# Kernel tuning notes

Hardware: AMD Instinct MI355X
Metric: run time of the kernel (lower is better)

## Reference

```python
import jax, jax.numpy as jnp
import numpy as np

B, LTMS, TTS, C_IN, F, H = 64, 16, 256, 128, 256, 256


def setup_inputs() -> dict:
    key = jax.random.key(0)
    ks = jax.random.split(key, 6)
    s = 0.05  # small init keeps relu-GRU numerically tame
    return {
        "x": jax.random.normal(ks[0], (B, LTMS * TTS, C_IN), dtype=jnp.float32),
        "conv_w": jax.random.normal(ks[1], (1, C_IN, F), dtype=jnp.float32) * s,
        "conv_b": jnp.zeros((F,), dtype=jnp.float32),
        "attn_w": jax.random.normal(ks[2], (TTS, TTS), dtype=jnp.float32) * s,
        "attn_b": jnp.zeros((TTS,), dtype=jnp.float32),
        "gru_w": jax.random.normal(ks[3], (F, 3 * H), dtype=jnp.float32) * s,
        "gru_u": jax.random.normal(ks[4], (H, 3 * H), dtype=jnp.float32) * s,
        "gru_b": jnp.zeros((2, 3 * H), dtype=jnp.float32),
    }


def _forward(x, conv_w, conv_b, attn_w, attn_b, gru_w, gru_u, gru_b):
    b = x.shape[0]
    # [B, LTMS*TTS, C] -> [B*LTMS, TTS, C]; segments are independent, so the
    # original per-segment Python loop vectorizes into the leading batch dim.
    xs = x.reshape(b * LTMS, TTS, C_IN)
    # Conv1D kernel_size=1 == pointwise GEMM, then ReLU (dropout=0 at inference)
    conv = jax.nn.relu(jnp.einsum('ntc,cf->ntf', xs, conv_w[0]) + conv_b)  # [N,T,F]
    # Attention: softmax(Dense) over time axis per filter, multiply back
    xt = conv.transpose(0, 2, 1)                                  # [N,F,T]
    probs = jax.nn.softmax(xt @ attn_w + attn_b, axis=-1)         # [N,F,T]
    x_att = conv * probs.transpose(0, 2, 1)                       # [N,T,F]
    # GRU (keras v2, reset_after=True), activation=relu, gate order z,r,h
    bi, br = gru_b[0], gru_b[1]
    gates_x = x_att @ gru_w + bi                                  # [N,T,3H]
    def step(h, gx):
        rec = h @ gru_u + br
        xz, xr, xh = jnp.split(gx, 3, axis=-1)
        rz, rr, rh = jnp.split(rec, 3, axis=-1)
        z = jax.nn.sigmoid(xz + rz)
        r = jax.nn.sigmoid(xr + rr)
        hh = jax.nn.relu(xh + r * rh)
        h_new = z * h + (1.0 - z) * hh
        return h_new, None
    h0 = jnp.zeros((b * LTMS, H), dtype=x.dtype)
    h_final, _ = jax.lax.scan(step, h0, gates_x.transpose(1, 0, 2))
    return h_final.reshape(b, LTMS, H)


def reference(x, conv_w, conv_b, attn_w, attn_b, gru_w, gru_u, gru_b):
    return _forward(x, conv_w, conv_b, attn_w, attn_b, gru_w, gru_u, gru_b)
```

## Files before the change

kernel.cpp:

```cpp
#include <hip/hip_runtime.h>
#include <stdint.h>

typedef unsigned short u16;
typedef __attribute__((ext_vector_type(8))) __bf16 bf16x8;
typedef __attribute__((ext_vector_type(4))) float f32x4;

#define TTS 256
#define NSEG 1024
#define TC 32

__device__ __forceinline__ u16 f2bf(float f) {
  union { float f; uint32_t u; } v; v.f = f;
  uint32_t r = v.u + 0x7fffu + ((v.u >> 16) & 1u);
  return (u16)(r >> 16);
}
__device__ __forceinline__ float bf2f(u16 h) {
  union { uint32_t u; float f; } v; v.u = ((uint32_t)h) << 16;
  return v.f;
}
__device__ __forceinline__ float sigm(float x) {
  return __builtin_amdgcn_rcpf(1.0f + __expf(-x));
}
__device__ __forceinline__ void gl16(const void* g, void* l) {
  __builtin_amdgcn_global_load_lds(
      (const __attribute__((address_space(1))) unsigned int*)g,
      (__attribute__((address_space(3))) unsigned int*)l, 16, 0, 0);
}

__global__ void k_transp(const float* __restrict__ in, u16* __restrict__ out, int R, int C) {
  int i = blockIdx.x * blockDim.x + threadIdx.x;
  if (i < R * C) {
    int r = i / C, c = i % C;
    out[(size_t)c * R + r] = f2bf(in[i]);
  }
}

template <bool RELU, bool STORE_T, int AMODE>
__global__ __launch_bounds__(512, 2) void k_gemm(
    const void* __restrict__ Av, const u16* __restrict__ Bt,
    const float* __restrict__ bias, u16* __restrict__ out, int K, int Nld, int t0) {
  __shared__ __attribute__((aligned(16))) u16 ldsA[2][4096];
  __shared__ __attribute__((aligned(16))) u16 ldsB[2][8192];
  const int tid  = threadIdx.x;
  const int w    = tid >> 6;
  const int lane = tid & 63;
  const int quad = lane >> 4;
  const int l16  = lane & 15;
  const int m0 = blockIdx.x * 128;
  const int n0 = blockIdx.y * 256;
  const int wm = w >> 2, wn = w & 3;
  const int arow = tid & 127, ac = tid >> 7;
  const float* Af = (const float*)Av;
  const u16*   Ax = (const u16*)Av;

  f32x4 acc[4][4];
#pragma unroll
  for (int i = 0; i < 4; i++)
#pragma unroll
    for (int j = 0; j < 4; j++) acc[i][j] = f32x4{0.f, 0.f, 0.f, 0.f};

  float4 p0, p1;
  if (AMODE == 0) {
    const float* p = Af + (size_t)(m0 + arow) * K + ac * 8;
    p0 = *(const float4*)p;
    p1 = *(const float4*)(p + 4);
  } else {
    int r = m0 + arow, kk = ac * 8;
    gl16(Ax + (size_t)(r >> 5) * 65536 + (size_t)(kk >> 6) * 16384 +
             (t0 + (r & 31)) * 64 + (kk & 63),
         &ldsA[0][tid * 8]);
  }
#pragma unroll
  for (int i = 0; i < 2; i++) {
    int idx = i * 512 + tid, brow = idx & 255, bc = idx >> 8;
    gl16(Bt + (size_t)(n0 + brow) * K + bc * 8, &ldsB[0][idx * 8]);
  }
  if (AMODE == 0) {
    *(ushort4*)&ldsA[0][tid * 8]     = ushort4{f2bf(p0.x), f2bf(p0.y), f2bf(p0.z), f2bf(p0.w)};
    *(ushort4*)&ldsA[0][tid * 8 + 4] = ushort4{f2bf(p1.x), f2bf(p1.y), f2bf(p1.z), f2bf(p1.w)};
  }
  __syncthreads();

  int cur = 0;
  for (int k0 = 0; k0 < K; k0 += 32) {
    const int kn = k0 + 32;
    const bool more = kn < K;
    float4 q0, q1;
    if (more) {
      if (AMODE == 0) {
        const float* p = Af + (size_t)(m0 + arow) * K + kn + ac * 8;
        q0 = *(const float4*)p;
        q1 = *(const float4*)(p + 4);
      } else {
        int r = m0 + arow, kk = kn + ac * 8;
        gl16(Ax + (size_t)(r >> 5) * 65536 + (size_t)(kk >> 6) * 16384 +
                 (t0 + (r & 31)) * 64 + (kk & 63),
             &ldsA[cur ^ 1][tid * 8]);
      }
#pragma unroll
      for (int i = 0; i < 2; i++) {
        int idx = i * 512 + tid, brow = idx & 255, bc = idx >> 8;
        gl16(Bt + (size_t)(n0 + brow) * K + kn + bc * 8, &ldsB[cur ^ 1][idx * 8]);
      }
    }
    bf16x8 a[4], b[4];
#pragma unroll
    for (int i = 0; i < 4; i++)
      a[i] = *(const bf16x8*)&ldsA[cur][(quad * 128 + wm * 64 + i * 16 + l16) * 8];
#pragma unroll
    for (int j = 0; j < 4; j++)
      b[j] = *(const bf16x8*)&ldsB[cur][(quad * 256 + wn * 64 + j * 16 + l16) * 8];
#pragma unroll
    for (int i = 0; i < 4; i++)
#pragma unroll
      for (int j = 0; j < 4; j++)
        acc[i][j] = __builtin_amdgcn_mfma_f32_16x16x32_bf16(a[i], b[j], acc[i][j], 0, 0, 0);
    if (AMODE == 0 && more) {
      *(ushort4*)&ldsA[cur ^ 1][tid * 8]     = ushort4{f2bf(q0.x), f2bf(q0.y), f2bf(q0.z), f2bf(q0.w)};
      *(ushort4*)&ldsA[cur ^ 1][tid * 8 + 4] = ushort4{f2bf(q1.x), f2bf(q1.y), f2bf(q1.z), f2bf(q1.w)};
    }
    __syncthreads();
    cur ^= 1;
  }

#pragma unroll
  for (int j = 0; j < 4; j++) {
    int col = n0 + wn * 64 + j * 16 + l16;
    float bv = bias[col];
#pragma unroll
    for (int i = 0; i < 4; i++) {
      int row0 = m0 + wm * 64 + i * 16 + quad * 4;
      if (STORE_T) {
        int nseg = row0 >> 8, tt0 = row0 & 255;
        ushort4 o;
        float v0 = acc[i][j][0] + bv, v1 = acc[i][j][1] + bv;
        float v2 = acc[i][j][2] + bv, v3 = acc[i][j][3] + bv;
        if (RELU) {
          v0 = fmaxf(v0, 0.f); v1 = fmaxf(v1, 0.f);
          v2 = fmaxf(v2, 0.f); v3 = fmaxf(v3, 0.f);
        }
        o.x = f2bf(v0); o.y = f2bf(v1); o.z = f2bf(v2); o.w = f2bf(v3);
        *(ushort4*)&out[(size_t)nseg * 65536 + (size_t)(col >> 6) * 16384 +
                        (col & 63) * 256 + tt0] = o;
      } else {
#pragma unroll
        for (int r = 0; r < 4; r++) {
          float v = acc[i][j][r] + bv;
          if (RELU) v = fmaxf(v, 0.f);
          out[(size_t)(row0 + r) * Nld + col] = f2bf(v);
        }
      }
    }
  }
}

__global__ __launch_bounds__(256, 4) void k_attn(
    u16* xac,
    const u16* __restrict__ Wt,
    const float* __restrict__ attn_b) {
  __shared__ u16 ldsC[16384];
  __shared__ float redmax[4][64];
  __shared__ float redsum[4][64];
  const int tid  = threadIdx.x;
  const int w    = tid >> 6;
  const int lane = tid & 63;
  const int quad = lane >> 4;
  const int l16  = lane & 15;
  const int seg = blockIdx.x;
  const int c4  = blockIdx.y;
  u16* reg = xac + (size_t)seg * 65536 + (size_t)c4 * 16384;

  {
    const int f = tid & 63, g = tid >> 6;
#pragma unroll
    for (int u = 0; u < 8; u++) {
      int tch = g * 8 + u;
      *(bf16x8*)&ldsC[(tch * 64 + f) * 8] =
          *(const bf16x8*)(reg + (size_t)f * 256 + tch * 8);
    }
  }
  __syncthreads();

  f32x4 acc[4][4];
#pragma unroll
  for (int i = 0; i < 4; i++)
#pragma unroll
    for (int j = 0; j < 4; j++) acc[i][j] = f32x4{0.f, 0.f, 0.f, 0.f};

#pragma unroll
  for (int s = 0; s < 8; s++) {
    int k0 = s * 32;
    bf16x8 a[4], b[4];
#pragma unroll
    for (int i = 0; i < 4; i++)
      a[i] = *(const bf16x8*)(Wt + (size_t)(w * 64 + i * 16 + l16) * 256 + k0 + quad * 8);
#pragma unroll
    for (int j = 0; j < 4; j++)
      b[j] = *(const bf16x8*)&ldsC[((s * 4 + quad) * 64 + j * 16 + l16) * 8];
#pragma unroll
    for (int i = 0; i < 4; i++)
#pragma unroll
      for (int j = 0; j < 4; j++)
        acc[i][j] = __builtin_amdgcn_mfma_f32_16x16x32_bf16(a[i], b[j], acc[i][j], 0, 0, 0);
  }

#pragma unroll
  for (int i = 0; i < 4; i++)
#pragma unroll
    for (int r = 0; r < 4; r++) {
      float ab = attn_b[w * 64 + i * 16 + quad * 4 + r];
#pragma unroll
      for (int j = 0; j < 4; j++) acc[i][j][r] += ab;
    }

  float lmax[4];
#pragma unroll
  for (int j = 0; j < 4; j++) {
    float m = -1e30f;
#pragma unroll
    for (int i = 0; i < 4; i++)
#pragma unroll
      for (int r = 0; r < 4; r++) m = fmaxf(m, acc[i][j][r]);
    m = fmaxf(m, __shfl_xor(m, 16));
    m = fmaxf(m, __shfl_xor(m, 32));
    lmax[j] = m;
  }
  if (quad == 0) {
#pragma unroll
    for (int j = 0; j < 4; j++) redmax[w][j * 16 + l16] = lmax[j];
  }
  __syncthreads();
  float gmax[4];
#pragma unroll
  for (int j = 0; j < 4; j++) {
    int c = j * 16 + l16;
    gmax[j] = fmaxf(fmaxf(redmax[0][c], redmax[1][c]), fmaxf(redmax[2][c], redmax[3][c]));
  }
  float lsum[4];
#pragma unroll
  for (int j = 0; j < 4; j++) {
    float sacc = 0.f;
#pragma unroll
    for (int i = 0; i < 4; i++)
#pragma unroll
      for (int r = 0; r < 4; r++) {
        float e = __expf(acc[i][j][r] - gmax[j]);
        acc[i][j][r] = e;
        sacc += e;
      }
    sacc += __shfl_xor(sacc, 16);
    sacc += __shfl_xor(sacc, 32);
    lsum[j] = sacc;
  }
  if (quad == 0) {
#pragma unroll
    for (int j = 0; j < 4; j++) redsum[w][j * 16 + l16] = lsum[j];
  }
  __syncthreads();
  float rinv[4];
#pragma unroll
  for (int j = 0; j < 4; j++) {
    int c = j * 16 + l16;
    rinv[j] = 1.0f / (redsum[0][c] + redsum[1][c] + redsum[2][c] + redsum[3][c]);
  }

#pragma unroll
  for (int i = 0; i < 4; i++) {
#pragma unroll
    for (int r = 0; r < 4; r++) {
      int tp = w * 64 + i * 16 + quad * 4 + r;
#pragma unroll
      for (int j = 0; j < 4; j++) {
        int fl = j * 16 + l16;
        float cv = bf2f(ldsC[((tp >> 3) * 64 + fl) * 8 + (tp & 7)]);
        float xa = acc[i][j][r] * rinv[j] * cv;
        reg[(size_t)tp * 64 + fl] = f2bf(xa);
      }
    }
  }
}

__global__ __launch_bounds__(512, 2) void k_scanc(
    const u16* __restrict__ gc,
    const u16* __restrict__ Ut,
    const float* __restrict__ br,
    float* __restrict__ hio,
    int init) {
  __shared__ u16 uls[65536];
  __shared__ u16 hb[2][16 * 264];
  const int tid  = threadIdx.x;
  const int w    = tid >> 6;
  const int lane = tid & 63;
  const int quad = lane >> 4;
  const int l16  = lane & 15;
  const int n0 = blockIdx.x * 16;
  const int cg[2] = {w, 8 + w};

#pragma unroll
  for (int j = 0; j < 2; j++)
#pragma unroll
    for (int s = 0; s < 8; s++)
      *(bf16x8*)&uls[w * 8192 + (j * 8 + s) * 512 + lane * 8] =
          *(const bf16x8*)(Ut + (size_t)(j * 256 + cg[1] * 16 + l16) * 256 + s * 32 + quad * 8);

  bf16x8 ur0[3][8], urh1[8];
#pragma unroll
  for (int g = 0; g < 3; g++)
#pragma unroll
    for (int s = 0; s < 8; s++)
      ur0[g][s] = *(const bf16x8*)(Ut + (size_t)(g * 256 + cg[0] * 16 + l16) * 256 + s * 32 + quad * 8);
#pragma unroll
  for (int s = 0; s < 8; s++)
    urh1[s] = *(const bf16x8*)(Ut + (size_t)(512 + cg[1] * 16 + l16) * 256 + s * 32 + quad * 8);

  float brZ[2], brR[2], brH[2];
#pragma unroll
  for (int grp = 0; grp < 2; grp++) {
    int c = cg[grp] * 16 + l16;
    brZ[grp] = br[c]; brR[grp] = br[256 + c]; brH[grp] = br[512 + c];
  }

  float hreg[2][4];
#pragma unroll
  for (int grp = 0; grp < 2; grp++)
#pragma unroll
    for (int r = 0; r < 4; r++)
      hreg[grp][r] = init ? 0.f
                          : hio[(size_t)(n0 + quad * 4 + r) * 256 + cg[grp] * 16 + l16];
  {
    int sg = tid >> 5, c0 = (tid & 31) * 8;
    if (init) {
      *(ushort4*)&hb[0][sg * 264 + c0]     = ushort4{0, 0, 0, 0};
      *(ushort4*)&hb[0][sg * 264 + c0 + 4] = ushort4{0, 0, 0, 0};
    } else {
      const float* hp = hio + (size_t)(n0 + sg) * 256 + c0;
      float4 h0 = *(const float4*)(hp), h1 = *(const float4*)(hp + 4);
      *(ushort4*)&hb[0][sg * 264 + c0]     = ushort4{f2bf(h0.x), f2bf(h0.y), f2bf(h0.z), f2bf(h0.w)};
      *(ushort4*)&hb[0][sg * 264 + c0 + 4] = ushort4{f2bf(h1.x), f2bf(h1.y), f2bf(h1.z), f2bf(h1.w)};
    }
  }
  const u16* gseg[4];
#pragma unroll
  for (int r = 0; r < 4; r++)
    gseg[r] = gc + (size_t)(n0 + quad * 4 + r) * TC * 768;
  __syncthreads();

  u16 gA[2][3][4], gB[2][3][4];

  auto load_g = [&](int tt, u16 (&gr)[2][3][4]) {
#pragma unroll
    for (int grp = 0; grp < 2; grp++)
#pragma unroll
      for (int g = 0; g < 3; g++)
#pragma unroll
        for (int r = 0; r < 4; r++)
          gr[grp][g][r] = gseg[r][tt * 768 + g * 256 + cg[grp] * 16 + l16];
  };

  auto step = [&](int tt, const u16 (&gcur)[2][3][4], u16 (&gnext)[2][3][4],
                  int CUR) {
    if (tt + 1 < TC) load_g(tt + 1, gnext);

    f32x4 acc[2][3];
#pragma unroll
    for (int grp = 0; grp < 2; grp++)
#pragma unroll
      for (int g = 0; g < 3; g++) acc[grp][g] = f32x4{0.f, 0.f, 0.f, 0.f};

#pragma unroll
    for (int s = 0; s < 8; s++) {
      bf16x8 ah = *(const bf16x8*)&hb[CUR][l16 * 264 + s * 32 + quad * 8];
#pragma unroll
      for (int g = 0; g < 3; g++)
        acc[0][g] = __builtin_amdgcn_mfma_f32_16x16x32_bf16(ah, ur0[g][s], acc[0][g], 0, 0, 0);
      bf16x8 uz  = *(const bf16x8*)&uls[w * 8192 + s * 512 + lane * 8];
      bf16x8 urr = *(const bf16x8*)&uls[w * 8192 + (8 + s) * 512 + lane * 8];
      acc[1][0] = __builtin_amdgcn_mfma_f32_16x16x32_bf16(ah, uz,      acc[1][0], 0, 0, 0);
      acc[1][1] = __builtin_amdgcn_mfma_f32_16x16x32_bf16(ah, urr,     acc[1][1], 0, 0, 0);
      acc[1][2] = __builtin_amdgcn_mfma_f32_16x16x32_bf16(ah, urh1[s], acc[1][2], 0, 0, 0);
    }

#pragma unroll
    for (int grp = 0; grp < 2; grp++)
#pragma unroll
      for (int r = 0; r < 4; r++) {
        float z  = sigm(acc[grp][0][r] + bf2f(gcur[grp][0][r]) + brZ[grp]);
        float rg = sigm(acc[grp][1][r] + bf2f(gcur[grp][1][r]) + brR[grp]);
        float hh = fmaxf(bf2f(gcur[grp][2][r]) + rg * (acc[grp][2][r] + brH[grp]), 0.f);
        float hn = z * hreg[grp][r] + (1.0f - z) * hh;
        hreg[grp][r] = hn;
        hb[CUR ^ 1][(quad * 4 + r) * 264 + cg[grp] * 16 + l16] = f2bf(hn);
      }
    __syncthreads();
  };

  load_g(0, gA);
  for (int t2 = 0; t2 < TC; t2 += 2) {
    step(t2,     gA, gB, 0);
    step(t2 + 1, gB, gA, 1);
  }

#pragma unroll
  for (int grp = 0; grp < 2; grp++)
#pragma unroll
    for (int r = 0; r < 4; r++)
      hio[(size_t)(n0 + quad * 4 + r) * 256 + cg[grp] * 16 + l16] = hreg[grp][r];
}

extern "C" void kernel_launch(void* const* d_in, const int* in_sizes, int n_in,
                              void* d_out, int out_size, void* d_ws, size_t ws_size,
                              hipStream_t stream) {
  (void)in_sizes; (void)n_in; (void)out_size;
  const float* x      = (const float*)d_in[0];
  const float* conv_w = (const float*)d_in[1];
  const float* conv_b = (const float*)d_in[2];
  const float* attn_w = (const float*)d_in[3];
  const float* attn_b = (const float*)d_in[4];
  const float* gru_w  = (const float*)d_in[5];
  const float* gru_u  = (const float*)d_in[6];
  const float* gru_b  = (const float*)d_in[7];

  const size_t NEEDED = 185532416;
  if (ws_size < NEEDED) return;
  char* ws = (char*)d_ws;
  u16* xac     = (u16*)(ws);
  u16* gatesC  = (u16*)(ws + 134217728);
  u16* conv_wT = (u16*)(ws + 184549376);
  u16* attn_wT = (u16*)(ws + 184614912);
  u16* gru_wT  = (u16*)(ws + 184745984);
  u16* gru_uT  = (u16*)(ws + 185139200);

  hipLaunchKernelGGL(k_transp, dim3(128), dim3(256), 0, stream, conv_w, conv_wT, 128, 256);
  hipLaunchKernelGGL(k_transp, dim3(256), dim3(256), 0, stream, attn_w, attn_wT, 256, 256);
  hipLaunchKernelGGL(k_transp, dim3(768), dim3(256), 0, stream, gru_w, gru_wT, 256, 768);
  hipLaunchKernelGGL(k_transp, dim3(768), dim3(256), 0, stream, gru_u, gru_uT, 256, 768);

  hipLaunchKernelGGL((k_gemm<true, true, 0>), dim3(2048, 1), dim3(512), 0, stream,
                     (const void*)x, conv_wT, conv_b, xac, 128, 0, 0);
  hipLaunchKernelGGL(k_attn, dim3(1024, 4), dim3(256), 0, stream,
                     xac, attn_wT, attn_b);
  for (int c = 0; c < 8; c++) {
    hipLaunchKernelGGL((k_gemm<false, false, 1>), dim3(256, 3), dim3(512), 0, stream,
                       (const void*)xac, gru_wT, gru_b, gatesC, 256, 768, c * TC);
    hipLaunchKernelGGL(k_scanc, dim3(64), dim3(512), 0, stream,
                       gatesC, gru_uT, gru_b + 768, (float*)d_out, c == 0 ? 1 : 0);
  }
}
```

Measured before the change: 1.227 ms.

## Keep all recurrent weights in registers, coalesce attention stores, merge transposes

The scan kernel now holds the whole recurrent weight slice (2x3x8 bf16x8 per lane) in registers instead of splitting it between registers and LDS. It also stores the hidden state in LDS in a layout matched to the MFMA operand, which removes the per-step LDS weight reads. The attention kernel stages its outputs through a small LDS tile so global writes go out as 16-byte vectors instead of scattered 2-byte stores. The four weight-transpose launches are merged into one. The cost is heavy register pressure in the scan kernel (launch bounds 512,1), which risks spills, plus lower occupancy in the attention kernel.

```diff
diff --git a/kernel.cpp b/kernel.cpp
--- a/kernel.cpp
+++ b/kernel.cpp
@@ -3,6 +3,7 @@
 
 typedef unsigned short u16;
 typedef __attribute__((ext_vector_type(8))) __bf16 bf16x8;
+typedef __attribute__((ext_vector_type(8))) u16 u16x8;
 typedef __attribute__((ext_vector_type(4))) float f32x4;
 
 #define TTS 256
@@ -27,8 +28,17 @@
       (__attribute__((address_space(3))) unsigned int*)l, 16, 0, 0);
 }
 
-__global__ void k_transp(const float* __restrict__ in, u16* __restrict__ out, int R, int C) {
-  int i = blockIdx.x * blockDim.x + threadIdx.x;
+__global__ void k_transp4(const float* __restrict__ cw, const float* __restrict__ aw,
+                          const float* __restrict__ gw, const float* __restrict__ gu,
+                          u16* __restrict__ cwT, u16* __restrict__ awT,
+                          u16* __restrict__ gwT, u16* __restrict__ guT) {
+  int b = blockIdx.x;
+  const float* in; u16* out; int R, C, base;
+  if (b < 128)       { in = cw; out = cwT; R = 128; C = 256; base = 0; }
+  else if (b < 384)  { in = aw; out = awT; R = 256; C = 256; base = 128; }
+  else if (b < 1152) { in = gw; out = gwT; R = 256; C = 768; base = 384; }
+  else               { in = gu; out = guT; R = 256; C = 768; base = 1152; }
+  int i = (b - base) * 256 + threadIdx.x;
   if (i < R * C) {
     int r = i / C, c = i % C;
     out[(size_t)c * R + r] = f2bf(in[i]);
@@ -154,13 +164,14 @@
   }
 }
 
-__global__ __launch_bounds__(256, 4) void k_attn(
+__global__ __launch_bounds__(256, 3) void k_attn(
     u16* xac,
     const u16* __restrict__ Wt,
     const float* __restrict__ attn_b) {
   __shared__ u16 ldsC[16384];
   __shared__ float redmax[4][64];
   __shared__ float redsum[4][64];
+  __shared__ __attribute__((aligned(16))) u16 xbuf[4][16][76];
   const int tid  = threadIdx.x;
   const int w    = tid >> 6;
   const int lane = tid & 63;
@@ -274,20 +285,25 @@
         int fl = j * 16 + l16;
         float cv = bf2f(ldsC[((tp >> 3) * 64 + fl) * 8 + (tp & 7)]);
         float xa = acc[i][j][r] * rinv[j] * cv;
-        reg[(size_t)tp * 64 + fl] = f2bf(xa);
-      }
-    }
-  }
-}
-
-__global__ __launch_bounds__(512, 2) void k_scanc(
+        xbuf[w][quad * 4 + r][fl] = f2bf(xa);
+      }
+    }
+    int rr = lane >> 2, oc = lane & 3;
+    u16x8 v0 = *(const u16x8*)&xbuf[w][rr][oc * 16];
+    u16x8 v1 = *(const u16x8*)&xbuf[w][rr][oc * 16 + 8];
+    int tpb = w * 64 + i * 16 + rr;
+    *(u16x8*)&reg[(size_t)tpb * 64 + oc * 16]     = v0;
+    *(u16x8*)&reg[(size_t)tpb * 64 + oc * 16 + 8] = v1;
+  }
+}
+
+__global__ __launch_bounds__(512, 1) void k_scan(
     const u16* __restrict__ gc,
     const u16* __restrict__ Ut,
     const float* __restrict__ br,
     float* __restrict__ hio,
     int init) {
-  __shared__ u16 uls[65536];
-  __shared__ u16 hb[2][16 * 264];
+  __shared__ __attribute__((aligned(16))) u16 hbT[2][4096];
   const int tid  = threadIdx.x;
   const int w    = tid >> 6;
   const int lane = tid & 63;
@@ -296,22 +312,14 @@
   const int n0 = blockIdx.x * 16;
   const int cg[2] = {w, 8 + w};
 
-#pragma unroll
-  for (int j = 0; j < 2; j++)
-#pragma unroll
-    for (int s = 0; s < 8; s++)
-      *(bf16x8*)&uls[w * 8192 + (j * 8 + s) * 512 + lane * 8] =
-          *(const bf16x8*)(Ut + (size_t)(j * 256 + cg[1] * 16 + l16) * 256 + s * 32 + quad * 8);
-
-  bf16x8 ur0[3][8], urh1[8];
-#pragma unroll
-  for (int g = 0; g < 3; g++)
-#pragma unroll
-    for (int s = 0; s < 8; s++)
-      ur0[g][s] = *(const bf16x8*)(Ut + (size_t)(g * 256 + cg[0] * 16 + l16) * 256 + s * 32 + quad * 8);
-#pragma unroll
-  for (int s = 0; s < 8; s++)
-    urh1[s] = *(const bf16x8*)(Ut + (size_t)(512 + cg[1] * 16 + l16) * 256 + s * 32 + quad * 8);
+  bf16x8 U[2][3][8];
+#pragma unroll
+  for (int grp = 0; grp < 2; grp++)
+#pragma unroll
+    for (int g = 0; g < 3; g++)
+#pragma unroll
+      for (int s = 0; s < 8; s++)
+        U[grp][g][s] = *(const bf16x8*)(Ut + (size_t)(g * 256 + cg[grp] * 16 + l16) * 256 + s * 32 + quad * 8);
 
   float brZ[2], brR[2], brH[2];
 #pragma unroll
@@ -324,21 +332,14 @@
 #pragma unroll
   for (int grp = 0; grp < 2; grp++)
 #pragma unroll
-    for (int r = 0; r < 4; r++)
+    for (int r = 0; r < 4; r++) {
       hreg[grp][r] = init ? 0.f
                           : hio[(size_t)(n0 + quad * 4 + r) * 256 + cg[grp] * 16 + l16];
-  {
-    int sg = tid >> 5, c0 = (tid & 31) * 8;
-    if (init) {
-      *(ushort4*)&hb[0][sg * 264 + c0]     = ushort4{0, 0, 0, 0};
-      *(ushort4*)&hb[0][sg * 264 + c0 + 4] = ushort4{0, 0, 0, 0};
-    } else {
-      const float* hp = hio + (size_t)(n0 + sg) * 256 + c0;
-      float4 h0 = *(const float4*)(hp), h1 = *(const float4*)(hp + 4);
-      *(ushort4*)&hb[0][sg * 264 + c0]     = ushort4{f2bf(h0.x), f2bf(h0.y), f2bf(h0.z), f2bf(h0.w)};
-      *(ushort4*)&hb[0][sg * 264 + c0 + 4] = ushort4{f2bf(h1.x), f2bf(h1.y), f2bf(h1.z), f2bf(h1.w)};
-    }
-  }
+      int c = cg[grp] * 16 + l16;
+      int seg = quad * 4 + r;
+      hbT[0][(c >> 5) * 512 + ((c >> 3) & 3) * 128 + seg * 8 + (c & 7)] = f2bf(hreg[grp][r]);
+    }
+
   const u16* gseg[4];
 #pragma unroll
   for (int r = 0; r < 4; r++)
@@ -346,7 +347,6 @@
   __syncthreads();
 
   u16 gA[2][3][4], gB[2][3][4];
-
   auto load_g = [&](int tt, u16 (&gr)[2][3][4]) {
 #pragma unroll
     for (int grp = 0; grp < 2; grp++)
@@ -358,7 +358,7 @@
   };
 
   auto step = [&](int tt, const u16 (&gcur)[2][3][4], u16 (&gnext)[2][3][4],
-                  int CUR) {
+                  const u16* hR, u16* hW) {
     if (tt + 1 < TC) load_g(tt + 1, gnext);
 
     f32x4 acc[2][3];
@@ -369,15 +369,12 @@
 
 #pragma unroll
     for (int s = 0; s < 8; s++) {
-      bf16x8 ah = *(const bf16x8*)&hb[CUR][l16 * 264 + s * 32 + quad * 8];
-#pragma unroll
-      for (int g = 0; g < 3; g++)
-        acc[0][g] = __builtin_amdgcn_mfma_f32_16x16x32_bf16(ah, ur0[g][s], acc[0][g], 0, 0, 0);
-      bf16x8 uz  = *(const bf16x8*)&uls[w * 8192 + s * 512 + lane * 8];
-      bf16x8 urr = *(const bf16x8*)&uls[w * 8192 + (8 + s) * 512 + lane * 8];
-      acc[1][0] = __builtin_amdgcn_mfma_f32_16x16x32_bf16(ah, uz,      acc[1][0], 0, 0, 0);
-      acc[1][1] = __builtin_amdgcn_mfma_f32_16x16x32_bf16(ah, urr,     acc[1][1], 0, 0, 0);
-      acc[1][2] = __builtin_amdgcn_mfma_f32_16x16x32_bf16(ah, urh1[s], acc[1][2], 0, 0, 0);
+      bf16x8 ah = *(const bf16x8*)&hR[s * 512 + quad * 128 + l16 * 8];
+#pragma unroll
+      for (int grp = 0; grp < 2; grp++)
+#pragma unroll
+        for (int g = 0; g < 3; g++)
+          acc[grp][g] = __builtin_amdgcn_mfma_f32_16x16x32_bf16(ah, U[grp][g][s], acc[grp][g], 0, 0, 0);
     }
 
 #pragma unroll
@@ -389,15 +386,17 @@
         float hh = fmaxf(bf2f(gcur[grp][2][r]) + rg * (acc[grp][2][r] + brH[grp]), 0.f);
         float hn = z * hreg[grp][r] + (1.0f - z) * hh;
         hreg[grp][r] = hn;
-        hb[CUR ^ 1][(quad * 4 + r) * 264 + cg[grp] * 16 + l16] = f2bf(hn);
+        int c = cg[grp] * 16 + l16;
+        int seg = quad * 4 + r;
+        hW[(c >> 5) * 512 + ((c >> 3) & 3) * 128 + seg * 8 + (c & 7)] = f2bf(hn);
       }
     __syncthreads();
   };
 
   load_g(0, gA);
   for (int t2 = 0; t2 < TC; t2 += 2) {
-    step(t2,     gA, gB, 0);
-    step(t2 + 1, gB, gA, 1);
+    step(t2,     gA, gB, hbT[0], hbT[1]);
+    step(t2 + 1, gB, gA, hbT[1], hbT[0]);
   }
 
 #pragma unroll
@@ -430,10 +429,8 @@
   u16* gru_wT  = (u16*)(ws + 184745984);
   u16* gru_uT  = (u16*)(ws + 185139200);
 
-  hipLaunchKernelGGL(k_transp, dim3(128), dim3(256), 0, stream, conv_w, conv_wT, 128, 256);
-  hipLaunchKernelGGL(k_transp, dim3(256), dim3(256), 0, stream, attn_w, attn_wT, 256, 256);
-  hipLaunchKernelGGL(k_transp, dim3(768), dim3(256), 0, stream, gru_w, gru_wT, 256, 768);
-  hipLaunchKernelGGL(k_transp, dim3(768), dim3(256), 0, stream, gru_u, gru_uT, 256, 768);
+  hipLaunchKernelGGL(k_transp4, dim3(1920), dim3(256), 0, stream,
+                     conv_w, attn_w, gru_w, gru_u, conv_wT, attn_wT, gru_wT, gru_uT);
 
   hipLaunchKernelGGL((k_gemm<true, true, 0>), dim3(2048, 1), dim3(512), 0, stream,
                      (const void*)x, conv_wT, conv_b, xac, 128, 0, 0);
@@ -442,7 +439,7 @@
   for (int c = 0; c < 8; c++) {
     hipLaunchKernelGGL((k_gemm<false, false, 1>), dim3(256, 3), dim3(512), 0, stream,
                        (const void*)xac, gru_wT, gru_b, gatesC, 256, 768, c * TC);
-    hipLaunchKernelGGL(k_scanc, dim3(64), dim3(512), 0, stream,
+    hipLaunchKernelGGL(k_scan, dim3(64), dim3(512), 0, stream,
                        gatesC, gru_uT, gru_b + 768, (float*)d_out, c == 0 ? 1 : 0);
   }
 }
```

After: 1.639 ms. 1.33x slower.
